# Kernel optimization log

Hardware: AMD Instinct MI355X
Metric: run time of the kernel (lower is better)

Reference implementation:

```python
import jax, jax.numpy as jnp
import numpy as np

G, N, E = 64, 2048, 32768      # graphs, nodes/graph, edges/graph
D, H, O, L = 128, 128, 2, 3    # node_dim, hid_dim, out_dim, max_layer
ALL = 500_000                  # global feature table rows


def setup_inputs() -> dict:
    key = jax.random.key(0)
    ks = jax.random.split(key, 12)
    s = 1.0 / np.sqrt(D)  # D == H so one scale suffices
    return {
        "all_features": jax.random.normal(ks[0], (ALL, D), jnp.float32),
        "feature_index": jax.random.randint(ks[1], (G, N), 0, ALL),
        "edge_index": jax.random.randint(ks[2], (G, 2, E), 0, N),
        "action": 2,  # uses action+1 = 3 GCN layers
        "lin_res_w": jax.random.normal(ks[3], (D, H), jnp.float32) * s,
        "lin_res_b": jnp.zeros((H,), jnp.float32),
        "gcn_w": jax.random.normal(ks[4], (L, H, H), jnp.float32) * s,
        "gcn_b": jnp.zeros((L, H), jnp.float32),
        "fc1_w": jax.random.normal(ks[5], (H, H), jnp.float32) * s,
        "fc1_b": jnp.zeros((H,), jnp.float32),
        "lin_w": jax.random.normal(ks[6], (H, O), jnp.float32) * s,
        "lin_b": jnp.zeros((O,), jnp.float32),
    }


def _gcn_conv(x, src, dst, W, b):
    """PyG GCNConv: add self-loops, symmetric deg^-1/2 norm, scatter-add."""
    n = x.shape[0]
    h = x @ W                                             # [N,H]
    loop = jnp.arange(n)
    src2 = jnp.concatenate([src, loop])
    dst2 = jnp.concatenate([dst, loop])
    deg = jax.ops.segment_sum(jnp.ones_like(dst2, dtype=h.dtype), dst2,
                              num_segments=n)             # >=1 via self-loops
    dinv = jax.lax.rsqrt(deg)
    coef = dinv[src2] * dinv[dst2]                        # [E+N]
    out = jax.ops.segment_sum(h[src2] * coef[:, None], dst2, num_segments=n)
    return out + b


def reference(all_features, feature_index, edge_index, action,
              lin_res_w, lin_res_b, gcn_w, gcn_b,
              fc1_w, fc1_b, lin_w, lin_b):
    n_layers = int(action) + 1

    def per_graph(feats, src, dst):
        # residual branch (dropout is identity in eval mode)
        x1 = jax.nn.relu(feats @ lin_res_w + lin_res_b)   # [N,H]
        x = feats
        for k in range(n_layers):
            x = jax.nn.relu(_gcn_conv(x, src, dst, gcn_w[k], gcn_b[k]))
        x = jax.nn.relu((x + x1) @ fc1_w + fc1_b)
        return jnp.mean(x, axis=0)                        # [H]

    feats = all_features[feature_index]                   # [G,N,D] gather
    target_feats = jax.vmap(per_graph)(feats, edge_index[:, 0], edge_index[:, 1])
    logits = target_feats @ lin_w + lin_b                 # [G,O]
    return jax.nn.log_softmax(logits, axis=1), logits
```

## Files before the change

### kernel.cpp

```cpp
#include <hip/hip_runtime.h>

#define G 64
#define N 2048
#define E 32768
#define GN (G*N)
#define PADR 36

typedef __attribute__((ext_vector_type(8))) short bf16x8;
typedef __attribute__((ext_vector_type(4))) float f32x4;

__device__ __forceinline__ float4 ld4(const float* p) { return *reinterpret_cast<const float4*>(p); }
__device__ __forceinline__ unsigned short f2bf(float x) {
    unsigned u = __float_as_uint(x);
    u += 0x7FFF + ((u >> 16) & 1);
    return (unsigned short)(u >> 16);
}
__device__ __forceinline__ unsigned pack2(float a, float b) {
    return (unsigned)f2bf(a) | ((unsigned)f2bf(b) << 16);
}
__device__ __forceinline__ float bflo(unsigned u) { return __uint_as_float(u << 16); }
__device__ __forceinline__ float bfhi(unsigned u) { return __uint_as_float(u & 0xFFFF0000u); }
__device__ __forceinline__ float bfs(short s) { return __uint_as_float(((unsigned)(unsigned short)s) << 16); }

__device__ __forceinline__ int swz(int bid, int chunk) { return (bid & 7) * chunk + (bid >> 3); }

__global__ __launch_bounds__(1024) void k_init(const int* __restrict__ ei,
        int* __restrict__ offs, float* __restrict__ dinv,
        const float* __restrict__ wres, const float* __restrict__ gw,
        const float* __restrict__ wfc, unsigned short* __restrict__ Wt,
        float* __restrict__ tgt) {
    int t = threadIdx.x;
    if (blockIdx.x == G + 40) {
        #pragma unroll
        for (int j = 0; j < 8; ++j) tgt[j*1024 + t] = 0.f;
        return;
    }
    if (blockIdx.x >= G) {
        if (t >= 256) return;
        int pb = blockIdx.x - G;
        int m = pb >> 3;
        int tid = (pb & 7) * 256 + t;
        const float* src = (m == 0) ? wres : (m < 4 ? gw + (size_t)(m-1)*16384 : wfc);
        int c = tid >> 4, q = tid & 15;
        float v[8];
        #pragma unroll
        for (int j = 0; j < 8; ++j) v[j] = src[(q*8 + j)*128 + c];
        uint4 p;
        p.x = pack2(v[0], v[1]); p.y = pack2(v[2], v[3]);
        p.z = pack2(v[4], v[5]); p.w = pack2(v[6], v[7]);
        *reinterpret_cast<uint4*>(Wt + (size_t)m*16384 + c*128 + ((q ^ (c & 7)) << 3)) = p;
        return;
    }
    int g = blockIdx.x;
    __shared__ int scnt[2048];
    __shared__ int swave[16];
    scnt[t] = 0; scnt[t + 1024] = 0;
    __syncthreads();
    const int* dstp = ei + (size_t)g*2*E + E;
    for (int e = t; e < E; e += 1024) atomicAdd(&scnt[dstp[e]], 1);
    __syncthreads();
    int a = scnt[2*t], b = scnt[2*t + 1];
    int s = a + b;
    int lane = t & 63, wid = t >> 6;
    #pragma unroll
    for (int d = 1; d < 64; d <<= 1) { int v = __shfl_up(s, d); if (lane >= d) s += v; }
    if (lane == 63) swave[wid] = s;
    __syncthreads();
    if (t < 16) {
        int v = swave[t];
        #pragma unroll
        for (int d = 1; d < 16; d <<= 1) { int u = __shfl_up(v, d); if (t >= d) v += u; }
        swave[t] = v;
    }
    __syncthreads();
    int woff = (wid == 0) ? 0 : swave[wid - 1];
    int e0 = woff + s - (a + b);
    int e1 = e0 + a;
    offs[g*(N+1) + 2*t]     = e0;
    offs[g*(N+1) + 2*t + 1] = e1;
    if (t == 0) offs[g*(N+1) + N] = E;
    dinv[(g<<11) + 2*t]     = rsqrtf((float)(a + 1));
    dinv[(g<<11) + 2*t + 1] = rsqrtf((float)(b + 1));
}

__global__ __launch_bounds__(512) void k_gemm_g2(const int* __restrict__ fidx,
        const float* __restrict__ tab, const unsigned short* __restrict__ Wt,
        const float* __restrict__ bres, const float* __restrict__ dinv,
        unsigned short* __restrict__ X1, unsigned short* __restrict__ Hb,
        const int* __restrict__ ei, const int* __restrict__ offs, int* __restrict__ adj) {
    __shared__ unsigned short sW[2*16384];
    const int t = threadIdx.x;

    if (blockIdx.x < G) {
        int* cur = reinterpret_cast<int*>(sW);
        int g = blockIdx.x;
        #pragma unroll
        for (int i = 0; i < 4; ++i) cur[i*512 + t] = offs[g*(N+1) + i*512 + t];
        __syncthreads();
        const int* srcp = ei + (size_t)g*2*E;
        const int* dstp = srcp + E;
        for (int e = t; e < E; e += 512) {
            int dst = dstp[e];
            int pos = atomicAdd(&cur[dst], 1);
            adj[(size_t)g*E + pos] = srcp[e];
        }
        return;
    }

    {
        const float4* s = reinterpret_cast<const float4*>(Wt);
        float4* d = reinterpret_cast<float4*>(sW);
        #pragma unroll
        for (int i = 0; i < 8; ++i) d[i*512 + t] = s[i*512 + t];
    }
    __syncthreads();

    const int lane = t & 63, w = t >> 6;
    const int wrow = (w & 3) << 6;
    const int wcol = (w >> 2) << 6;
    const size_t row0 = (size_t)swz(blockIdx.x - G, GN/256/8) * 256;
    const int l15 = lane & 15, l4 = lane >> 4;

    size_t rbase[4];
    const float* rowp[4];
    #pragma unroll
    for (int f2 = 0; f2 < 4; ++f2) {
        rbase[f2] = row0 + wrow + f2*16 + l15;
        rowp[f2] = tab + (size_t)fidx[rbase[f2]] * 128;
    }

    f32x4 acc0[4][4], acc1[4][4];
    #pragma unroll
    for (int i = 0; i < 4; ++i)
        #pragma unroll
        for (int j = 0; j < 4; ++j) {
            acc0[i][j] = (f32x4){0.f, 0.f, 0.f, 0.f};
            acc1[i][j] = (f32x4){0.f, 0.f, 0.f, 0.f};
        }

    #pragma unroll
    for (int kk = 0; kk < 4; ++kk) {
        bf16x8 xf[4];
        #pragma unroll
        for (int f2 = 0; f2 < 4; ++f2) {
            int col = (kk << 5) + (l4 << 3);
            float4 u = ld4(rowp[f2] + col);
            float4 v = ld4(rowp[f2] + col + 4);
            bf16x8 r;
            r[0] = (short)f2bf(u.x); r[1] = (short)f2bf(u.y);
            r[2] = (short)f2bf(u.z); r[3] = (short)f2bf(u.w);
            r[4] = (short)f2bf(v.x); r[5] = (short)f2bf(v.y);
            r[6] = (short)f2bf(v.z); r[7] = (short)f2bf(v.w);
            xf[f2] = r;
        }
        #pragma unroll
        for (int f = 0; f < 4; ++f) {
            int c = wcol + f*16 + l15;
            int off = c*128 + (((kk*4 + l4) ^ (c & 7)) << 3);
            bf16x8 wf0 = *reinterpret_cast<const bf16x8*>(&sW[off]);
            bf16x8 wf1 = *reinterpret_cast<const bf16x8*>(&sW[16384 + off]);
            #pragma unroll
            for (int f2 = 0; f2 < 4; ++f2) {
                acc0[f2][f] = __builtin_amdgcn_mfma_f32_16x16x32_bf16(wf0, xf[f2], acc0[f2][f], 0, 0, 0);
                acc1[f2][f] = __builtin_amdgcn_mfma_f32_16x16x32_bf16(wf1, xf[f2], acc1[f2][f], 0, 0, 0);
            }
        }
    }

    float dv[4];
    #pragma unroll
    for (int f2 = 0; f2 < 4; ++f2) dv[f2] = dinv[rbase[f2]];

    #pragma unroll
    for (int f = 0; f < 4; ++f) {
        int colb = wcol + f*16 + (l4 << 2);
        float4 bs = ld4(bres + colb);
        #pragma unroll
        for (int f2 = 0; f2 < 4; ++f2) {
            f32x4 v0 = acc0[f2][f];
            uint2 p0;
            p0.x = pack2(fmaxf(v0[0] + bs.x, 0.f), fmaxf(v0[1] + bs.y, 0.f));
            p0.y = pack2(fmaxf(v0[2] + bs.z, 0.f), fmaxf(v0[3] + bs.w, 0.f));
            *reinterpret_cast<uint2*>(X1 + (rbase[f2] << 7) + colb) = p0;
            f32x4 v1 = acc1[f2][f];
            float d = dv[f2];
            uint2 p1;
            p1.x = pack2(v1[0]*d, v1[1]*d);
            p1.y = pack2(v1[2]*d, v1[3]*d);
            *reinterpret_cast<uint2*>(Hb + (rbase[f2] << 7) + colb) = p1;
        }
    }
}

template<int MODE>
__global__ __launch_bounds__(512) void k_gemm(const unsigned short* __restrict__ A,
        const unsigned short* __restrict__ A2, const unsigned short* __restrict__ Wt,
        const float* __restrict__ bias, const float* __restrict__ dinv,
        unsigned short* __restrict__ C, float* __restrict__ tgt) {
    __shared__ unsigned short sW[16384];
    const int t = threadIdx.x;
    {
        const float4* s = reinterpret_cast<const float4*>(Wt);
        float4* d = reinterpret_cast<float4*>(sW);
        #pragma unroll
        for (int i = 0; i < 4; ++i) d[i*512 + t] = s[i*512 + t];
    }
    __syncthreads();

    const int lane = t & 63, w = t >> 6;
    const int wrow = (w & 3) << 6;
    const int wcol = (w >> 2) << 6;
    const size_t row0 = (size_t)swz(blockIdx.x, GN/256/8) * 256;
    const int l15 = lane & 15, l4 = lane >> 4;

    size_t rbase[4];
    #pragma unroll
    for (int f2 = 0; f2 < 4; ++f2) rbase[f2] = row0 + wrow + f2*16 + l15;

    f32x4 acc[4][4];
    #pragma unroll
    for (int i = 0; i < 4; ++i)
        #pragma unroll
        for (int j = 0; j < 4; ++j) acc[i][j] = (f32x4){0.f, 0.f, 0.f, 0.f};

    #pragma unroll
    for (int kk = 0; kk < 4; ++kk) {
        bf16x8 xf[4];
        #pragma unroll
        for (int f2 = 0; f2 < 4; ++f2) {
            const unsigned short* ap = A + (rbase[f2] << 7) + (kk << 5) + (l4 << 3);
            if (MODE == 2) {
                bf16x8 x = *reinterpret_cast<const bf16x8*>(ap);
                bf16x8 y = *reinterpret_cast<const bf16x8*>(A2 + (rbase[f2] << 7) + (kk << 5) + (l4 << 3));
                bf16x8 r;
                #pragma unroll
                for (int j = 0; j < 8; ++j) r[j] = (short)f2bf(bfs(x[j]) + bfs(y[j]));
                xf[f2] = r;
            } else {
                xf[f2] = *reinterpret_cast<const bf16x8*>(ap);
            }
        }
        #pragma unroll
        for (int f = 0; f < 4; ++f) {
            int c = wcol + f*16 + l15;
            int off = c*128 + (((kk*4 + l4) ^ (c & 7)) << 3);
            bf16x8 wf = *reinterpret_cast<const bf16x8*>(&sW[off]);
            #pragma unroll
            for (int f2 = 0; f2 < 4; ++f2)
                acc[f2][f] = __builtin_amdgcn_mfma_f32_16x16x32_bf16(wf, xf[f2], acc[f2][f], 0, 0, 0);
        }
    }

    if (MODE == 2) {
        float cs[4][4];
        #pragma unroll
        for (int f = 0; f < 4; ++f) {
            int colb = wcol + f*16 + (l4 << 2);
            float4 bs = ld4(bias + colb);
            #pragma unroll
            for (int j = 0; j < 4; ++j) cs[f][j] = 0.f;
            #pragma unroll
            for (int f2 = 0; f2 < 4; ++f2) {
                cs[f][0] += fmaxf(acc[f2][f][0] + bs.x, 0.f);
                cs[f][1] += fmaxf(acc[f2][f][1] + bs.y, 0.f);
                cs[f][2] += fmaxf(acc[f2][f][2] + bs.z, 0.f);
                cs[f][3] += fmaxf(acc[f2][f][3] + bs.w, 0.f);
            }
        }
        #pragma unroll
        for (int d = 1; d < 16; d <<= 1)
            #pragma unroll
            for (int f = 0; f < 4; ++f)
                #pragma unroll
                for (int j = 0; j < 4; ++j)
                    cs[f][j] += __shfl_xor(cs[f][j], d);
        if (l15 == 0) {
            int g = (int)(row0 >> 11);
            #pragma unroll
            for (int f = 0; f < 4; ++f)
                #pragma unroll
                for (int j = 0; j < 4; ++j)
                    atomicAdd(&tgt[g*128 + wcol + f*16 + (l4 << 2) + j], cs[f][j]);
        }
        return;
    }

    float dv[4];
    #pragma unroll
    for (int f2 = 0; f2 < 4; ++f2) dv[f2] = dinv[rbase[f2]];
    #pragma unroll
    for (int f = 0; f < 4; ++f) {
        int colb = wcol + f*16 + (l4 << 2);
        #pragma unroll
        for (int f2 = 0; f2 < 4; ++f2) {
            f32x4 v = acc[f2][f];
            float d = dv[f2];
            uint2 p; p.x = pack2(v[0]*d, v[1]*d); p.y = pack2(v[2]*d, v[3]*d);
            *reinterpret_cast<uint2*>(C + (rbase[f2] << 7) + colb) = p;
        }
    }
}

__global__ __launch_bounds__(1024) void k_agg(const unsigned short* __restrict__ h,
        const int* __restrict__ adj, const int* __restrict__ offs,
        const float* __restrict__ dinv, const float* __restrict__ bias,
        unsigned short* __restrict__ out) {
    __shared__ unsigned short sIN[2048 * PADR];
    const int t = threadIdx.x;
    const int g  = blockIdx.x >> 2;
    const int c0 = (blockIdx.x & 3) << 5;
    const unsigned short* hg = h + (((size_t)g << 11) << 7) + c0;

    {
        int r0 = t >> 3;
        int j  = t & 7;
        for (int i = 0; i < 16; ++i) {
            int r = r0 + (i << 7);
            uint2 v = *reinterpret_cast<const uint2*>(hg + ((size_t)r << 7) + j*4);
            *reinterpret_cast<uint2*>(&sIN[r*PADR + j*4]) = v;
        }
    }
    __syncthreads();

    const int* al = adj + (size_t)g*E;
    float bs[32];
    #pragma unroll
    for (int q = 0; q < 8; ++q) {
        float4 b4 = ld4(bias + c0 + q*4);
        bs[q*4] = b4.x; bs[q*4+1] = b4.y; bs[q*4+2] = b4.z; bs[q*4+3] = b4.w;
    }

    #pragma unroll
    for (int i = 0; i < 2; ++i) {
        int n = t + (i << 10);
        int st = offs[g*(N+1) + n];
        int en = offs[g*(N+1) + n + 1];
        float acc[32];
        {
            const unsigned short* rp = &sIN[n*PADR];
            #pragma unroll
            for (int q = 0; q < 8; ++q) {
                uint2 u = *reinterpret_cast<const uint2*>(rp + q*4);
                acc[q*4]   = bflo(u.x); acc[q*4+1] = bfhi(u.x);
                acc[q*4+2] = bflo(u.y); acc[q*4+3] = bfhi(u.y);
            }
        }
        int e = st;
        for (; e + 2 <= en; e += 2) {
            int s0 = al[e], s1 = al[e+1];
            const unsigned short* rp0 = &sIN[s0*PADR];
            const unsigned short* rp1 = &sIN[s1*PADR];
            uint2 u0[8], u1[8];
            #pragma unroll
            for (int q = 0; q < 8; ++q) u0[q] = *reinterpret_cast<const uint2*>(rp0 + q*4);
            #pragma unroll
            for (int q = 0; q < 8; ++q) u1[q] = *reinterpret_cast<const uint2*>(rp1 + q*4);
            #pragma unroll
            for (int q = 0; q < 8; ++q) {
                acc[q*4]   += bflo(u0[q].x) + bflo(u1[q].x);
                acc[q*4+1] += bfhi(u0[q].x) + bfhi(u1[q].x);
                acc[q*4+2] += bflo(u0[q].y) + bflo(u1[q].y);
                acc[q*4+3] += bfhi(u0[q].y) + bfhi(u1[q].y);
            }
        }
        if (e < en) {
            const unsigned short* rp = &sIN[al[e]*PADR];
            #pragma unroll
            for (int q = 0; q < 8; ++q) {
                uint2 u = *reinterpret_cast<const uint2*>(rp + q*4);
                acc[q*4]   += bflo(u.x); acc[q*4+1] += bfhi(u.x);
                acc[q*4+2] += bflo(u.y); acc[q*4+3] += bfhi(u.y);
            }
        }
        float d = dinv[(g << 11) + n];
        unsigned short* op = out + (((size_t)(g << 11) + n) << 7) + c0;
        uint4 o0, o1;
        o0.x = pack2(fmaxf(acc[0]*d+bs[0],0.f),  fmaxf(acc[1]*d+bs[1],0.f));
        o0.y = pack2(fmaxf(acc[2]*d+bs[2],0.f),  fmaxf(acc[3]*d+bs[3],0.f));
        o0.z = pack2(fmaxf(acc[4]*d+bs[4],0.f),  fmaxf(acc[5]*d+bs[5],0.f));
        o0.w = pack2(fmaxf(acc[6]*d+bs[6],0.f),  fmaxf(acc[7]*d+bs[7],0.f));
        o1.x = pack2(fmaxf(acc[8]*d+bs[8],0.f),  fmaxf(acc[9]*d+bs[9],0.f));
        o1.y = pack2(fmaxf(acc[10]*d+bs[10],0.f),fmaxf(acc[11]*d+bs[11],0.f));
        o1.z = pack2(fmaxf(acc[12]*d+bs[12],0.f),fmaxf(acc[13]*d+bs[13],0.f));
        o1.w = pack2(fmaxf(acc[14]*d+bs[14],0.f),fmaxf(acc[15]*d+bs[15],0.f));
        *reinterpret_cast<uint4*>(op) = o0;
        *reinterpret_cast<uint4*>(op + 8) = o1;
        uint4 o2, o3;
        o2.x = pack2(fmaxf(acc[16]*d+bs[16],0.f),fmaxf(acc[17]*d+bs[17],0.f));
        o2.y = pack2(fmaxf(acc[18]*d+bs[18],0.f),fmaxf(acc[19]*d+bs[19],0.f));
        o2.z = pack2(fmaxf(acc[20]*d+bs[20],0.f),fmaxf(acc[21]*d+bs[21],0.f));
        o2.w = pack2(fmaxf(acc[22]*d+bs[22],0.f),fmaxf(acc[23]*d+bs[23],0.f));
        o3.x = pack2(fmaxf(acc[24]*d+bs[24],0.f),fmaxf(acc[25]*d+bs[25],0.f));
        o3.y = pack2(fmaxf(acc[26]*d+bs[26],0.f),fmaxf(acc[27]*d+bs[27],0.f));
        o3.z = pack2(fmaxf(acc[28]*d+bs[28],0.f),fmaxf(acc[29]*d+bs[29],0.f));
        o3.w = pack2(fmaxf(acc[30]*d+bs[30],0.f),fmaxf(acc[31]*d+bs[31],0.f));
        *reinterpret_cast<uint4*>(op + 16) = o2;
        *reinterpret_cast<uint4*>(op + 24) = o3;
    }
}

__global__ __launch_bounds__(64) void k_final(const float* __restrict__ tgt,
        const float* __restrict__ lw, const float* __restrict__ lb, float* __restrict__ outp) {
    int g = blockIdx.x, lane = threadIdx.x;
    float l0 = 0.f, l1 = 0.f;
    #pragma unroll
    for (int c = lane; c < 128; c += 64) {
        float v = tgt[g*128 + c] * (1.0f/2048.0f);
        l0 += v * lw[c*2];
        l1 += v * lw[c*2 + 1];
    }
    #pragma unroll
    for (int d = 32; d; d >>= 1) { l0 += __shfl_xor(l0, d); l1 += __shfl_xor(l1, d); }
    if (lane == 0) {
        l0 += lb[0]; l1 += lb[1];
        float m = fmaxf(l0, l1);
        float lse = m + logf(expf(l0 - m) + expf(l1 - m));
        outp[g*2]         = l0 - lse;
        outp[g*2 + 1]     = l1 - lse;
        outp[G*2 + g*2]     = l0;
        outp[G*2 + g*2 + 1] = l1;
    }
}

extern "C" void kernel_launch(void* const* d_in, const int* in_sizes, int n_in,
                              void* d_out, int out_size, void* d_ws, size_t ws_size,
                              hipStream_t stream) {
    const float* all_features = (const float*)d_in[0];
    const int*   fidx = (const int*)d_in[1];
    const int*   ei   = (const int*)d_in[2];
    const float* wres = (const float*)d_in[4];
    const float* bres = (const float*)d_in[5];
    const float* gw   = (const float*)d_in[6];
    const float* gb   = (const float*)d_in[7];
    const float* wfc  = (const float*)d_in[8];
    const float* bfc  = (const float*)d_in[9];
    const float* lw   = (const float*)d_in[10];
    const float* lb   = (const float*)d_in[11];
    float* out = (float*)d_out;

    char* ws = (char*)d_ws;
    size_t o = 0;
    auto alloc = [&](size_t bytes) { char* p = ws + o; o += (bytes + 255) & ~(size_t)255; return p; };
    unsigned short* X  = (unsigned short*)alloc((size_t)GN*128*2);
    unsigned short* Hb = (unsigned short*)alloc((size_t)GN*128*2);
    unsigned short* X1 = (unsigned short*)alloc((size_t)GN*128*2);
    unsigned short* Wt = (unsigned short*)alloc((size_t)5*16384*2);
    int*   adj  = (int*)alloc((size_t)G*E*4);
    int*   offs = (int*)alloc((size_t)G*(N+1)*4);
    float* dinv = (float*)alloc((size_t)GN*4);
    float* tgt  = (float*)alloc((size_t)G*128*4);

    k_init<<<G + 41, 1024, 0, stream>>>(ei, offs, dinv, wres, gw, wfc, Wt, tgt);

    k_gemm_g2<<<G + GN/256, 512, 0, stream>>>(fidx, all_features, Wt, bres, dinv, X1, Hb,
                                              ei, offs, adj);

    k_agg<<<G*4, 1024, 0, stream>>>(Hb, adj, offs, dinv, gb, X);
    for (int l = 1; l < 3; ++l) {
        k_gemm<1><<<GN/256, 512, 0, stream>>>(X, nullptr, Wt + (size_t)(1+l)*16384, nullptr, dinv, Hb, nullptr);
        k_agg<<<G*4, 1024, 0, stream>>>(Hb, adj, offs, dinv, gb + (size_t)l*128, X);
    }

    k_gemm<2><<<GN/256, 512, 0, stream>>>(X, X1, Wt + (size_t)4*16384, bfc, nullptr, nullptr, tgt);

    k_final<<<G, 64, 0, stream>>>(tgt, lw, lb, out);
}
```

Measured before the change: 292.2 us.

## Degree-sort nodes in aggregation and widen LDS row loads to 128-bit

k_init now builds a per-graph counting-sort permutation of nodes by in-degree (capped at 63), and k_agg processes nodes in that order. Threads in a wavefront then get similar edge counts, which cuts divergence in the per-node neighbor loop. The LDS row padding grows from 36 to 40 so rows are 16-byte aligned, letting every shared-memory read become a uint4 instead of a uint2. The costs are an extra indirection per node, scattered output writes, and a changed LDS bank pattern.

```diff
diff --git a/kernel.cpp b/kernel.cpp
--- a/kernel.cpp
+++ b/kernel.cpp
@@ -4,7 +4,7 @@
 #define N 2048
 #define E 32768
 #define GN (G*N)
-#define PADR 36
+#define PADR 40
 
 typedef __attribute__((ext_vector_type(8))) short bf16x8;
 typedef __attribute__((ext_vector_type(4))) float f32x4;
@@ -25,7 +25,7 @@
 __device__ __forceinline__ int swz(int bid, int chunk) { return (bid & 7) * chunk + (bid >> 3); }
 
 __global__ __launch_bounds__(1024) void k_init(const int* __restrict__ ei,
-        int* __restrict__ offs, float* __restrict__ dinv,
+        int* __restrict__ offs, float* __restrict__ dinv, int* __restrict__ perm,
         const float* __restrict__ wres, const float* __restrict__ gw,
         const float* __restrict__ wfc, unsigned short* __restrict__ Wt,
         float* __restrict__ tgt) {
@@ -54,7 +54,9 @@
     int g = blockIdx.x;
     __shared__ int scnt[2048];
     __shared__ int swave[16];
+    __shared__ int hist[64];
     scnt[t] = 0; scnt[t + 1024] = 0;
+    if (t < 64) hist[t] = 0;
     __syncthreads();
     const int* dstp = ei + (size_t)g*2*E + E;
     for (int e = t; e < E; e += 1024) atomicAdd(&scnt[dstp[e]], 1);
@@ -81,6 +83,22 @@
     if (t == 0) offs[g*(N+1) + N] = E;
     dinv[(g<<11) + 2*t]     = rsqrtf((float)(a + 1));
     dinv[(g<<11) + 2*t + 1] = rsqrtf((float)(b + 1));
+    int ba = min(a, 63), bb = min(b, 63);
+    atomicAdd(&hist[ba], 1);
+    atomicAdd(&hist[bb], 1);
+    __syncthreads();
+    if (t < 64) {
+        int v = hist[t];
+        int inc = v;
+        #pragma unroll
+        for (int d = 1; d < 64; d <<= 1) { int u = __shfl_up(inc, d); if (t >= d) inc += u; }
+        hist[t] = inc - v;
+    }
+    __syncthreads();
+    int sa = atomicAdd(&hist[ba], 1);
+    perm[(g<<11) + sa] = 2*t;
+    int sb = atomicAdd(&hist[bb], 1);
+    perm[(g<<11) + sb] = 2*t + 1;
 }
 
 __global__ __launch_bounds__(512) void k_gemm_g2(const int* __restrict__ fidx,
@@ -303,6 +321,7 @@
 
 __global__ __launch_bounds__(1024) void k_agg(const unsigned short* __restrict__ h,
         const int* __restrict__ adj, const int* __restrict__ offs,
+        const int* __restrict__ perm,
         const float* __restrict__ dinv, const float* __restrict__ bias,
         unsigned short* __restrict__ out) {
     __shared__ unsigned short sIN[2048 * PADR];
@@ -332,17 +351,19 @@
 
     #pragma unroll
     for (int i = 0; i < 2; ++i) {
-        int n = t + (i << 10);
+        int n = perm[(g << 11) + t + (i << 10)];
         int st = offs[g*(N+1) + n];
         int en = offs[g*(N+1) + n + 1];
         float acc[32];
         {
             const unsigned short* rp = &sIN[n*PADR];
             #pragma unroll
-            for (int q = 0; q < 8; ++q) {
-                uint2 u = *reinterpret_cast<const uint2*>(rp + q*4);
-                acc[q*4]   = bflo(u.x); acc[q*4+1] = bfhi(u.x);
-                acc[q*4+2] = bflo(u.y); acc[q*4+3] = bfhi(u.y);
+            for (int k = 0; k < 4; ++k) {
+                uint4 u = *reinterpret_cast<const uint4*>(rp + k*8);
+                acc[k*8]   = bflo(u.x); acc[k*8+1] = bfhi(u.x);
+                acc[k*8+2] = bflo(u.y); acc[k*8+3] = bfhi(u.y);
+                acc[k*8+4] = bflo(u.z); acc[k*8+5] = bfhi(u.z);
+                acc[k*8+6] = bflo(u.w); acc[k*8+7] = bfhi(u.w);
             }
         }
         int e = st;
@@ -350,26 +371,32 @@
             int s0 = al[e], s1 = al[e+1];
             const unsigned short* rp0 = &sIN[s0*PADR];
             const unsigned short* rp1 = &sIN[s1*PADR];
-            uint2 u0[8], u1[8];
-            #pragma unroll
-            for (int q = 0; q < 8; ++q) u0[q] = *reinterpret_cast<const uint2*>(rp0 + q*4);
-            #pragma unroll
-            for (int q = 0; q < 8; ++q) u1[q] = *reinterpret_cast<const uint2*>(rp1 + q*4);
-            #pragma unroll
-            for (int q = 0; q < 8; ++q) {
-                acc[q*4]   += bflo(u0[q].x) + bflo(u1[q].x);
-                acc[q*4+1] += bfhi(u0[q].x) + bfhi(u1[q].x);
-                acc[q*4+2] += bflo(u0[q].y) + bflo(u1[q].y);
-                acc[q*4+3] += bfhi(u0[q].y) + bfhi(u1[q].y);
+            uint4 u0[4], u1[4];
+            #pragma unroll
+            for (int k = 0; k < 4; ++k) u0[k] = *reinterpret_cast<const uint4*>(rp0 + k*8);
+            #pragma unroll
+            for (int k = 0; k < 4; ++k) u1[k] = *reinterpret_cast<const uint4*>(rp1 + k*8);
+            #pragma unroll
+            for (int k = 0; k < 4; ++k) {
+                acc[k*8]   += bflo(u0[k].x) + bflo(u1[k].x);
+                acc[k*8+1] += bfhi(u0[k].x) + bfhi(u1[k].x);
+                acc[k*8+2] += bflo(u0[k].y) + bflo(u1[k].y);
+                acc[k*8+3] += bfhi(u0[k].y) + bfhi(u1[k].y);
+                acc[k*8+4] += bflo(u0[k].z) + bflo(u1[k].z);
+                acc[k*8+5] += bfhi(u0[k].z) + bfhi(u1[k].z);
+                acc[k*8+6] += bflo(u0[k].w) + bflo(u1[k].w);
+                acc[k*8+7] += bfhi(u0[k].w) + bfhi(u1[k].w);
             }
         }
         if (e < en) {
             const unsigned short* rp = &sIN[al[e]*PADR];
             #pragma unroll
-            for (int q = 0; q < 8; ++q) {
-                uint2 u = *reinterpret_cast<const uint2*>(rp + q*4);
-                acc[q*4]   += bflo(u.x); acc[q*4+1] += bfhi(u.x);
-                acc[q*4+2] += bflo(u.y); acc[q*4+3] += bfhi(u.y);
+            for (int k = 0; k < 4; ++k) {
+                uint4 u = *reinterpret_cast<const uint4*>(rp + k*8);
+                acc[k*8]   += bflo(u.x); acc[k*8+1] += bfhi(u.x);
+                acc[k*8+2] += bflo(u.y); acc[k*8+3] += bfhi(u.y);
+                acc[k*8+4] += bflo(u.z); acc[k*8+5] += bfhi(u.z);
+                acc[k*8+6] += bflo(u.w); acc[k*8+7] += bfhi(u.w);
             }
         }
         float d = dinv[(g << 11) + n];
@@ -447,18 +474,19 @@
     unsigned short* Wt = (unsigned short*)alloc((size_t)5*16384*2);
     int*   adj  = (int*)alloc((size_t)G*E*4);
     int*   offs = (int*)alloc((size_t)G*(N+1)*4);
+    int*   perm = (int*)alloc((size_t)GN*4);
     float* dinv = (float*)alloc((size_t)GN*4);
     float* tgt  = (float*)alloc((size_t)G*128*4);
 
-    k_init<<<G + 41, 1024, 0, stream>>>(ei, offs, dinv, wres, gw, wfc, Wt, tgt);
+    k_init<<<G + 41, 1024, 0, stream>>>(ei, offs, dinv, perm, wres, gw, wfc, Wt, tgt);
 
     k_gemm_g2<<<G + GN/256, 512, 0, stream>>>(fidx, all_features, Wt, bres, dinv, X1, Hb,
                                               ei, offs, adj);
 
-    k_agg<<<G*4, 1024, 0, stream>>>(Hb, adj, offs, dinv, gb, X);
+    k_agg<<<G*4, 1024, 0, stream>>>(Hb, adj, offs, perm, dinv, gb, X);
     for (int l = 1; l < 3; ++l) {
         k_gemm<1><<<GN/256, 512, 0, stream>>>(X, nullptr, Wt + (size_t)(1+l)*16384, nullptr, dinv, Hb, nullptr);
-        k_agg<<<G*4, 1024, 0, stream>>>(Hb, adj, offs, dinv, gb + (size_t)l*128, X);
+        k_agg<<<G*4, 1024, 0, stream>>>(Hb, adj, offs, perm, dinv, gb + (size_t)l*128, X);
     }
 
     k_gemm<2><<<GN/256, 512, 0, stream>>>(X, X1, Wt + (size_t)4*16384, bfc, nullptr, nullptr, tgt);
```

Result: no change. 287.0 us (-1.8%).

## Replace CSR adjacency with degree-sorted jagged-diagonal layout for aggregation

Applied to the files above, without the earlier changes.

Nodes are bucketed by in-degree and sorted in descending order, and the adjacency is stored level by level (jagged diagonal / ELL style). Each aggregation thread handles one sorted row, so neighbor-index loads across a wavefront become contiguous and lanes in a wavefront have similar degrees. This targets uncoalesced index reads and divergent loop trip counts in the aggregation kernel. In exchange it adds histogram and permutation work to the init kernel plus extra perm/sdeg/sdinv loads. The level table has only 128 entries, so it silently assumes every in-degree is below 128.

```diff
diff --git a/kernel.cpp b/kernel.cpp
--- a/kernel.cpp
+++ b/kernel.cpp
@@ -25,7 +25,8 @@
 __device__ __forceinline__ int swz(int bid, int chunk) { return (bid & 7) * chunk + (bid >> 3); }
 
 __global__ __launch_bounds__(1024) void k_init(const int* __restrict__ ei,
-        int* __restrict__ offs, float* __restrict__ dinv,
+        float* __restrict__ dinv, int* __restrict__ perm, int* __restrict__ rankg,
+        int* __restrict__ sdeg, float* __restrict__ sdinv, int* __restrict__ lvlG,
         const float* __restrict__ wres, const float* __restrict__ gw,
         const float* __restrict__ wfc, unsigned short* __restrict__ Wt,
         float* __restrict__ tgt) {
@@ -53,56 +54,73 @@
     }
     int g = blockIdx.x;
     __shared__ int scnt[2048];
-    __shared__ int swave[16];
+    __shared__ int hist[128];
+    __shared__ int basev[129];
+    __shared__ int lvl[128];
+    __shared__ int ctr[128];
     scnt[t] = 0; scnt[t + 1024] = 0;
+    if (t < 128) { hist[t] = 0; ctr[t] = 0; }
     __syncthreads();
     const int* dstp = ei + (size_t)g*2*E + E;
     for (int e = t; e < E; e += 1024) atomicAdd(&scnt[dstp[e]], 1);
     __syncthreads();
     int a = scnt[2*t], b = scnt[2*t + 1];
-    int s = a + b;
-    int lane = t & 63, wid = t >> 6;
-    #pragma unroll
-    for (int d = 1; d < 64; d <<= 1) { int v = __shfl_up(s, d); if (lane >= d) s += v; }
-    if (lane == 63) swave[wid] = s;
-    __syncthreads();
-    if (t < 16) {
-        int v = swave[t];
-        #pragma unroll
-        for (int d = 1; d < 16; d <<= 1) { int u = __shfl_up(v, d); if (t >= d) v += u; }
-        swave[t] = v;
-    }
-    __syncthreads();
-    int woff = (wid == 0) ? 0 : swave[wid - 1];
-    int e0 = woff + s - (a + b);
-    int e1 = e0 + a;
-    offs[g*(N+1) + 2*t]     = e0;
-    offs[g*(N+1) + 2*t + 1] = e1;
-    if (t == 0) offs[g*(N+1) + N] = E;
     dinv[(g<<11) + 2*t]     = rsqrtf((float)(a + 1));
     dinv[(g<<11) + 2*t + 1] = rsqrtf((float)(b + 1));
+    int ba = min(a, 127), bb = min(b, 127);
+    atomicAdd(&hist[ba], 1);
+    atomicAdd(&hist[bb], 1);
+    __syncthreads();
+    if (t == 0) {
+        int suf = 0;
+        basev[128] = 0;
+        for (int d = 127; d >= 0; --d) { suf += hist[d]; basev[d] = suf; }
+        int run = 0;
+        for (int i = 0; i < 128; ++i) { lvl[i] = run; run += basev[i + 1]; }
+    }
+    __syncthreads();
+    {
+        int sa = basev[ba + 1] + atomicAdd(&ctr[ba], 1);
+        perm[(g<<11) + sa] = 2*t;
+        sdeg[(g<<11) + sa] = a;
+        sdinv[(g<<11) + sa] = rsqrtf((float)(a + 1));
+        rankg[(g<<11) + 2*t] = sa;
+        int sb = basev[bb + 1] + atomicAdd(&ctr[bb], 1);
+        perm[(g<<11) + sb] = 2*t + 1;
+        sdeg[(g<<11) + sb] = b;
+        sdinv[(g<<11) + sb] = rsqrtf((float)(b + 1));
+        rankg[(g<<11) + 2*t + 1] = sb;
+    }
+    if (t < 128) lvlG[g*128 + t] = lvl[t];
 }
 
 __global__ __launch_bounds__(512) void k_gemm_g2(const int* __restrict__ fidx,
         const float* __restrict__ tab, const unsigned short* __restrict__ Wt,
         const float* __restrict__ bres, const float* __restrict__ dinv,
         unsigned short* __restrict__ X1, unsigned short* __restrict__ Hb,
-        const int* __restrict__ ei, const int* __restrict__ offs, int* __restrict__ adj) {
+        const int* __restrict__ ei, const int* __restrict__ rankg,
+        const int* __restrict__ lvlG, int* __restrict__ padj) {
     __shared__ unsigned short sW[2*16384];
     const int t = threadIdx.x;
 
     if (blockIdx.x < G) {
-        int* cur = reinterpret_cast<int*>(sW);
+        int* cur   = reinterpret_cast<int*>(sW);
+        int* rankL = cur + 2048;
+        int* lvlL  = rankL + 2048;
         int g = blockIdx.x;
         #pragma unroll
-        for (int i = 0; i < 4; ++i) cur[i*512 + t] = offs[g*(N+1) + i*512 + t];
+        for (int i = 0; i < 4; ++i) {
+            cur[i*512 + t] = 0;
+            rankL[i*512 + t] = rankg[(g<<11) + i*512 + t];
+        }
+        if (t < 128) lvlL[t] = lvlG[g*128 + t];
         __syncthreads();
         const int* srcp = ei + (size_t)g*2*E;
         const int* dstp = srcp + E;
         for (int e = t; e < E; e += 512) {
             int dst = dstp[e];
-            int pos = atomicAdd(&cur[dst], 1);
-            adj[(size_t)g*E + pos] = srcp[e];
+            int i = atomicAdd(&cur[dst], 1);
+            padj[(size_t)g*E + lvlL[i] + rankL[dst]] = srcp[e];
         }
         return;
     }
@@ -302,15 +320,18 @@
 }
 
 __global__ __launch_bounds__(1024) void k_agg(const unsigned short* __restrict__ h,
-        const int* __restrict__ adj, const int* __restrict__ offs,
-        const float* __restrict__ dinv, const float* __restrict__ bias,
+        const int* __restrict__ padj, const int* __restrict__ lvlG,
+        const int* __restrict__ perm, const int* __restrict__ sdeg,
+        const float* __restrict__ sdinv, const float* __restrict__ bias,
         unsigned short* __restrict__ out) {
     __shared__ unsigned short sIN[2048 * PADR];
+    __shared__ int lvlL[128];
     const int t = threadIdx.x;
     const int g  = blockIdx.x >> 2;
     const int c0 = (blockIdx.x & 3) << 5;
     const unsigned short* hg = h + (((size_t)g << 11) << 7) + c0;
 
+    if (t < 128) lvlL[t] = lvlG[g*128 + t];
     {
         int r0 = t >> 3;
         int j  = t & 7;
@@ -322,7 +343,7 @@
     }
     __syncthreads();
 
-    const int* al = adj + (size_t)g*E;
+    const int* pa = padj + (size_t)g*E;
     float bs[32];
     #pragma unroll
     for (int q = 0; q < 8; ++q) {
@@ -331,10 +352,11 @@
     }
 
     #pragma unroll
-    for (int i = 0; i < 2; ++i) {
-        int n = t + (i << 10);
-        int st = offs[g*(N+1) + n];
-        int en = offs[g*(N+1) + n + 1];
+    for (int half = 0; half < 2; ++half) {
+        const int r = t + (half << 10);
+        const int n  = perm[(g << 11) + r];
+        const int dg = sdeg[(g << 11) + r];
+        const float dv = sdinv[(g << 11) + r];
         float acc[32];
         {
             const unsigned short* rp = &sIN[n*PADR];
@@ -345,9 +367,10 @@
                 acc[q*4+2] = bflo(u.y); acc[q*4+3] = bfhi(u.y);
             }
         }
-        int e = st;
-        for (; e + 2 <= en; e += 2) {
-            int s0 = al[e], s1 = al[e+1];
+        int i = 0;
+        for (; i + 2 <= dg; i += 2) {
+            int s0 = pa[lvlL[i] + r];
+            int s1 = pa[lvlL[i+1] + r];
             const unsigned short* rp0 = &sIN[s0*PADR];
             const unsigned short* rp1 = &sIN[s1*PADR];
             uint2 u0[8], u1[8];
@@ -363,8 +386,9 @@
                 acc[q*4+3] += bfhi(u0[q].y) + bfhi(u1[q].y);
             }
         }
-        if (e < en) {
-            const unsigned short* rp = &sIN[al[e]*PADR];
+        if (i < dg) {
+            int s = pa[lvlL[i] + r];
+            const unsigned short* rp = &sIN[s*PADR];
             #pragma unroll
             for (int q = 0; q < 8; ++q) {
                 uint2 u = *reinterpret_cast<const uint2*>(rp + q*4);
@@ -372,28 +396,27 @@
                 acc[q*4+2] += bflo(u.y); acc[q*4+3] += bfhi(u.y);
             }
         }
-        float d = dinv[(g << 11) + n];
         unsigned short* op = out + (((size_t)(g << 11) + n) << 7) + c0;
         uint4 o0, o1;
-        o0.x = pack2(fmaxf(acc[0]*d+bs[0],0.f),  fmaxf(acc[1]*d+bs[1],0.f));
-        o0.y = pack2(fmaxf(acc[2]*d+bs[2],0.f),  fmaxf(acc[3]*d+bs[3],0.f));
-        o0.z = pack2(fmaxf(acc[4]*d+bs[4],0.f),  fmaxf(acc[5]*d+bs[5],0.f));
-        o0.w = pack2(fmaxf(acc[6]*d+bs[6],0.f),  fmaxf(acc[7]*d+bs[7],0.f));
-        o1.x = pack2(fmaxf(acc[8]*d+bs[8],0.f),  fmaxf(acc[9]*d+bs[9],0.f));
-        o1.y = pack2(fmaxf(acc[10]*d+bs[10],0.f),fmaxf(acc[11]*d+bs[11],0.f));
-        o1.z = pack2(fmaxf(acc[12]*d+bs[12],0.f),fmaxf(acc[13]*d+bs[13],0.f));
-        o1.w = pack2(fmaxf(acc[14]*d+bs[14],0.f),fmaxf(acc[15]*d+bs[15],0.f));
+        o0.x = pack2(fmaxf(acc[0]*dv+bs[0],0.f),  fmaxf(acc[1]*dv+bs[1],0.f));
+        o0.y = pack2(fmaxf(acc[2]*dv+bs[2],0.f),  fmaxf(acc[3]*dv+bs[3],0.f));
+        o0.z = pack2(fmaxf(acc[4]*dv+bs[4],0.f),  fmaxf(acc[5]*dv+bs[5],0.f));
+        o0.w = pack2(fmaxf(acc[6]*dv+bs[6],0.f),  fmaxf(acc[7]*dv+bs[7],0.f));
+        o1.x = pack2(fmaxf(acc[8]*dv+bs[8],0.f),  fmaxf(acc[9]*dv+bs[9],0.f));
+        o1.y = pack2(fmaxf(acc[10]*dv+bs[10],0.f),fmaxf(acc[11]*dv+bs[11],0.f));
+        o1.z = pack2(fmaxf(acc[12]*dv+bs[12],0.f),fmaxf(acc[13]*dv+bs[13],0.f));
+        o1.w = pack2(fmaxf(acc[14]*dv+bs[14],0.f),fmaxf(acc[15]*dv+bs[15],0.f));
         *reinterpret_cast<uint4*>(op) = o0;
         *reinterpret_cast<uint4*>(op + 8) = o1;
         uint4 o2, o3;
-        o2.x = pack2(fmaxf(acc[16]*d+bs[16],0.f),fmaxf(acc[17]*d+bs[17],0.f));
-        o2.y = pack2(fmaxf(acc[18]*d+bs[18],0.f),fmaxf(acc[19]*d+bs[19],0.f));
-        o2.z = pack2(fmaxf(acc[20]*d+bs[20],0.f),fmaxf(acc[21]*d+bs[21],0.f));
-        o2.w = pack2(fmaxf(acc[22]*d+bs[22],0.f),fmaxf(acc[23]*d+bs[23],0.f));
-        o3.x = pack2(fmaxf(acc[24]*d+bs[24],0.f),fmaxf(acc[25]*d+bs[25],0.f));
-        o3.y = pack2(fmaxf(acc[26]*d+bs[26],0.f),fmaxf(acc[27]*d+bs[27],0.f));
-        o3.z = pack2(fmaxf(acc[28]*d+bs[28],0.f),fmaxf(acc[29]*d+bs[29],0.f));
-        o3.w = pack2(fmaxf(acc[30]*d+bs[30],0.f),fmaxf(acc[31]*d+bs[31],0.f));
+        o2.x = pack2(fmaxf(acc[16]*dv+bs[16],0.f),fmaxf(acc[17]*dv+bs[17],0.f));
+        o2.y = pack2(fmaxf(acc[18]*dv+bs[18],0.f),fmaxf(acc[19]*dv+bs[19],0.f));
+        o2.z = pack2(fmaxf(acc[20]*dv+bs[20],0.f),fmaxf(acc[21]*dv+bs[21],0.f));
+        o2.w = pack2(fmaxf(acc[22]*dv+bs[22],0.f),fmaxf(acc[23]*dv+bs[23],0.f));
+        o3.x = pack2(fmaxf(acc[24]*dv+bs[24],0.f),fmaxf(acc[25]*dv+bs[25],0.f));
+        o3.y = pack2(fmaxf(acc[26]*dv+bs[26],0.f),fmaxf(acc[27]*dv+bs[27],0.f));
+        o3.z = pack2(fmaxf(acc[28]*dv+bs[28],0.f),fmaxf(acc[29]*dv+bs[29],0.f));
+        o3.w = pack2(fmaxf(acc[30]*dv+bs[30],0.f),fmaxf(acc[31]*dv+bs[31],0.f));
         *reinterpret_cast<uint4*>(op + 16) = o2;
         *reinterpret_cast<uint4*>(op + 24) = o3;
     }
@@ -445,20 +468,25 @@
     unsigned short* Hb = (unsigned short*)alloc((size_t)GN*128*2);
     unsigned short* X1 = (unsigned short*)alloc((size_t)GN*128*2);
     unsigned short* Wt = (unsigned short*)alloc((size_t)5*16384*2);
-    int*   adj  = (int*)alloc((size_t)G*E*4);
-    int*   offs = (int*)alloc((size_t)G*(N+1)*4);
-    float* dinv = (float*)alloc((size_t)GN*4);
-    float* tgt  = (float*)alloc((size_t)G*128*4);
-
-    k_init<<<G + 41, 1024, 0, stream>>>(ei, offs, dinv, wres, gw, wfc, Wt, tgt);
+    int*   padj  = (int*)alloc((size_t)G*E*4);
+    int*   lvlG  = (int*)alloc((size_t)G*128*4);
+    int*   perm  = (int*)alloc((size_t)GN*4);
+    int*   rankg = (int*)alloc((size_t)GN*4);
+    int*   sdeg  = (int*)alloc((size_t)GN*4);
+    float* sdinv = (float*)alloc((size_t)GN*4);
+    float* dinv  = (float*)alloc((size_t)GN*4);
+    float* tgt   = (float*)alloc((size_t)G*128*4);
+
+    k_init<<<G + 41, 1024, 0, stream>>>(ei, dinv, perm, rankg, sdeg, sdinv, lvlG,
+                                        wres, gw, wfc, Wt, tgt);
 
     k_gemm_g2<<<G + GN/256, 512, 0, stream>>>(fidx, all_features, Wt, bres, dinv, X1, Hb,
-                                              ei, offs, adj);
-
-    k_agg<<<G*4, 1024, 0, stream>>>(Hb, adj, offs, dinv, gb, X);
+                                              ei, rankg, lvlG, padj);
+
+    k_agg<<<G*4, 1024, 0, stream>>>(Hb, padj, lvlG, perm, sdeg, sdinv, gb, X);
     for (int l = 1; l < 3; ++l) {
         k_gemm<1><<<GN/256, 512, 0, stream>>>(X, nullptr, Wt + (size_t)(1+l)*16384, nullptr, dinv, Hb, nullptr);
-        k_agg<<<G*4, 1024, 0, stream>>>(Hb, adj, offs, dinv, gb + (size_t)l*128, X);
+        k_agg<<<G*4, 1024, 0, stream>>>(Hb, padj, lvlG, perm, sdeg, sdinv, gb + (size_t)l*128, X);
     }
 
     k_gemm<2><<<GN/256, 512, 0, stream>>>(X, X1, Wt + (size_t)4*16384, bfc, nullptr, nullptr, tgt);
```

Result: faster. 268.8 us (-8.0%).
